# Kernel tuning notes

Measured on AMD Instinct MI355X. Metric: run time of the kernel, lower is better.

The kernel has to match this reference:

```python
import jax, jax.numpy as jnp
import numpy as np

IN_DIM, EDGE_DIM, HID = 128, 64, 128
N_A, N_B, E_AB, E_AA = 50000, 50000, 320000, 320000


def setup_inputs() -> dict:
    key = jax.random.key(0)
    ks = jax.random.split(key, 13)
    inv = lambda n: 1.0 / np.sqrt(n)
    return {
        "x_a": jax.random.normal(ks[0], (N_A, IN_DIM), jnp.float32),
        "x_b": jax.random.normal(ks[1], (N_B, IN_DIM), jnp.float32),
        "ei_ab": jax.random.randint(ks[2], (2, E_AB), 0, N_A),
        "ea_ab": jax.random.normal(ks[3], (E_AB, EDGE_DIM), jnp.float32),
        "ei_aa": jax.random.randint(ks[4], (2, E_AA), 0, N_A),
        "ea_aa": jax.random.normal(ks[5], (E_AA, EDGE_DIM), jnp.float32),
        "Wh_w": jax.random.normal(ks[6], (EDGE_DIM, HID), jnp.float32) * inv(EDGE_DIM),
        "Wh_b": jnp.zeros((HID,), jnp.float32),
        "Wn_w": jax.random.normal(ks[7], (2 * IN_DIM, HID), jnp.float32) * inv(2 * IN_DIM),
        "Wn_b": jnp.zeros((HID,), jnp.float32),
        "w_e": jax.random.normal(ks[8], (HID,), jnp.float32) * inv(HID),
        "ft_w": jax.random.normal(ks[9], (IN_DIM, IN_DIM), jnp.float32) * inv(IN_DIM),
        "ft_b": jnp.zeros((IN_DIM,), jnp.float32),
    }


def reference(x_a, x_b, ei_ab, ea_ab, ei_aa, ea_aa,
              Wh_w, Wh_b, Wn_w, Wn_b, w_e, ft_w, ft_b):
    def edge_alpha(x_src, x_dst, ei, ea):
        # gather src/dst feats -> linear + relu -> score -> softmax over all edges
        s, d = ei[0], ei[1]
        nf = jnp.concatenate([x_src[s], x_dst[d]], axis=1)          # [E, 2*in_dim]
        h = jax.nn.relu(ea @ Wh_w + Wh_b + nf @ Wn_w + Wn_b)         # [E, hid]
        return jax.nn.softmax(h @ w_e, axis=0)                       # [E]

    alpha_ab = edge_alpha(x_a, x_b, ei_ab, ea_ab)
    alpha_aa = edge_alpha(x_a, x_a, ei_aa, ea_aa)

    lf_a = jnp.zeros_like(x_a)
    lf_b = jnp.zeros_like(x_b)
    s_ab, d_ab = ei_ab[0], ei_ab[1]
    # cross-type edge: scatter into both endpoint node types
    lf_a = lf_a.at[s_ab].add(-alpha_ab[:, None] * x_b[d_ab])
    lf_b = lf_b.at[d_ab].add(-alpha_ab[:, None] * x_a[s_ab])
    s_aa, d_aa = ei_aa[0], ei_aa[1]
    # same-type edge: single scatter (src side only, per original)
    lf_a = lf_a.at[s_aa].add(-alpha_aa[:, None] * x_a[d_aa])

    out_a = x_a + lf_a
    out_a = out_a + (out_a @ ft_w + ft_b)
    out_b = x_b + lf_b
    out_b = out_b + (out_b @ ft_w + ft_b)
    return out_a, out_b, alpha_ab, alpha_aa
```

## Files before the change

### kernel.cpp

```cpp
#include <hip/hip_runtime.h>
#include <hip/hip_fp16.h>
#include <cstdint>
#include <cstddef>

#define N_A   50000
#define N_B   50000
#define E_AB  320000
#define E_AA  320000
#define IN_DIM 128
#define HID    128
#define ED     64

using bf16x8 = __attribute__((ext_vector_type(8))) short;
using f32x4  = __attribute__((ext_vector_type(4))) float;
typedef unsigned short ushort_t;
typedef unsigned int   uint_t;
typedef unsigned char  uchar_t;

#define X8_SCALE 0.0625f

__device__ inline ushort_t bf16r(float f) {
    uint_t u = __float_as_uint(f);
    u = (u + 0x7FFF + ((u >> 16) & 1)) >> 16;
    return (ushort_t)u;
}
__device__ inline float bf2f(ushort_t h) {
    return __uint_as_float(((uint_t)h) << 16);
}
__device__ inline ushort_t f16r(float f) { return __half_as_ushort(__float2half_rn(f)); }
__device__ inline float f16f(ushort_t u) { return __half2float(__ushort_as_half(u)); }
__device__ inline uint_t packh2(float a, float b) {
    return (uint_t)f16r(a) | ((uint_t)f16r(b) << 16);
}

__device__ inline uint_t enc_entry(int src, int flag, float score) {
    const uint_t h = (uint_t)f16r(score);
    return (uint_t)src | ((uint_t)flag << 16) | ((h & 0xFFFEu) << 16);
}

__device__ inline void online_merge(float& m, float& l, float om, float ol) {
    const float nm = fmaxf(m, om);
    l = l * __expf(m - nm) + ol * __expf(om - nm);
    m = nm;
}

__device__ inline uint_t pack_i8x4(float a, float b, float c, float d) {
    int q0 = __float2int_rn(a * 16.f); q0 = q0 < -127 ? -127 : (q0 > 127 ? 127 : q0);
    int q1 = __float2int_rn(b * 16.f); q1 = q1 < -127 ? -127 : (q1 > 127 ? 127 : q1);
    int q2 = __float2int_rn(c * 16.f); q2 = q2 < -127 ? -127 : (q2 > 127 ? 127 : q2);
    int q3 = __float2int_rn(d * 16.f); q3 = q3 < -127 ? -127 : (q3 > 127 ? 127 : q3);
    return (uint_t)(q0 & 0xFF) | ((uint_t)(q1 & 0xFF) << 8)
         | ((uint_t)(q2 & 0xFF) << 16) | ((uint_t)(q3 & 0xFF) << 24);
}

__global__ __launch_bounds__(64) void prep_w_all(
    const float* __restrict__ Wh, const float* __restrict__ W1,
    const float* __restrict__ W2, const float* __restrict__ FT,
    const float* __restrict__ we,
    ushort_t* __restrict__ BhWh, ushort_t* __restrict__ BlWh,
    ushort_t* __restrict__ BhW1, ushort_t* __restrict__ BlW1,
    ushort_t* __restrict__ BhW2, ushort_t* __restrict__ BlW2,
    ushort_t* __restrict__ BhFT, ushort_t* __restrict__ BlFT,
    float* __restrict__ wep)
{
    const int f = blockIdx.x;
    const int lane = threadIdx.x;
    if (f == 112) {
#pragma unroll
        for (int q = 0; q < 2; ++q) {
            const int idx = lane + q * 64;
            const int l15 = idx >> 3, ct = idx & 7;
            wep[idx] = we[ct * 16 + l15];
        }
        return;
    }
    const float* W; ushort_t *oh, *ol; int KT, fl;
    if (f < 16)      { W = Wh; oh = BhWh; ol = BlWh; KT = 2; fl = f; }
    else if (f < 48) { W = W1; oh = BhW1; ol = BlW1; KT = 4; fl = f - 16; }
    else if (f < 80) { W = W2; oh = BhW2; ol = BlW2; KT = 4; fl = f - 48; }
    else             { W = FT; oh = BhFT; ol = BlFT; KT = 4; fl = f - 80; }
    const int ct = fl / KT, kt = fl % KT;
    const int col = ct * 16 + (lane & 15);
    const int kb  = kt * 32 + (lane >> 4) * 8;
#pragma unroll
    for (int j = 0; j < 8; ++j) {
        const float v = W[(kb + j) * 128 + col];
        const ushort_t h = bf16r(v);
        oh[(size_t)(fl * 64 + lane) * 8 + j] = h;
        ol[(size_t)(fl * 64 + lane) * 8 + j] = bf16r(v - bf2f(h));
    }
}

__global__ __launch_bounds__(256) void proj_all_mfma(
    const float* __restrict__ x_a, const float* __restrict__ x_b,
    const ushort_t* __restrict__ B1h, const ushort_t* __restrict__ B1l,
    const ushort_t* __restrict__ B2h, const ushort_t* __restrict__ B2l,
    const float* __restrict__ bh, const float* __restrict__ bn,
    ushort_t* __restrict__ P1, ushort_t* __restrict__ P2a,
    ushort_t* __restrict__ P2b,
    uchar_t* __restrict__ xa8, uchar_t* __restrict__ xb8,
    int nblkA)
{
    const int lane = threadIdx.x & 63;
    const int l15 = lane & 15, lg = lane >> 4;
    const int isA = (blockIdx.x < nblkA);
    const int bb  = isA ? blockIdx.x : (blockIdx.x - nblkA);
    const int r0  = bb * 64 + (threadIdx.x >> 6) * 16;
    const int N   = isA ? N_A : N_B;
    const float* __restrict__ X = isA ? x_a : x_b;
    uchar_t* __restrict__ X8    = isA ? xa8 : xb8;
    const int arow = (r0 + l15 < N) ? (r0 + l15) : (N - 1);

    bf16x8 ahi[4], alo[4];
#pragma unroll
    for (int kt = 0; kt < 4; ++kt) {
        float v[8];
        *(float4*)(v + 0) = *(const float4*)&X[(size_t)arow * 128 + kt * 32 + lg * 8];
        *(float4*)(v + 4) = *(const float4*)&X[(size_t)arow * 128 + kt * 32 + lg * 8 + 4];
        uint2 xu;
        xu.x = pack_i8x4(v[0], v[1], v[2], v[3]);
        xu.y = pack_i8x4(v[4], v[5], v[6], v[7]);
        *(uint2*)&X8[(size_t)arow * 128 + kt * 32 + lg * 8] = xu;
#pragma unroll
        for (int j = 0; j < 8; ++j) {
            const ushort_t h = bf16r(v[j]);
            ahi[kt][j] = (short)h;
            alo[kt][j] = (short)bf16r(v[j] - bf2f(h));
        }
    }

    if (isA) {
        f32x4 acc1[8], acc2[8];
#pragma unroll
        for (int ct = 0; ct < 8; ++ct) {
            const float b = bh[ct * 16 + l15] + bn[ct * 16 + l15];
            acc1[ct] = (f32x4){b, b, b, b};
            acc2[ct] = (f32x4){0.f, 0.f, 0.f, 0.f};
        }
#pragma unroll
        for (int ct = 0; ct < 8; ++ct) {
#pragma unroll
            for (int kt = 0; kt < 4; ++kt) {
                const size_t fo = (size_t)((ct * 4 + kt) * 64 + lane) * 8;
                const bf16x8 b1h = *(const bf16x8*)&B1h[fo];
                const bf16x8 b1l = *(const bf16x8*)&B1l[fo];
                const bf16x8 b2h = *(const bf16x8*)&B2h[fo];
                const bf16x8 b2l = *(const bf16x8*)&B2l[fo];
                acc1[ct] = __builtin_amdgcn_mfma_f32_16x16x32_bf16(ahi[kt], b1h, acc1[ct], 0, 0, 0);
                acc1[ct] = __builtin_amdgcn_mfma_f32_16x16x32_bf16(alo[kt], b1h, acc1[ct], 0, 0, 0);
                acc1[ct] = __builtin_amdgcn_mfma_f32_16x16x32_bf16(ahi[kt], b1l, acc1[ct], 0, 0, 0);
                acc2[ct] = __builtin_amdgcn_mfma_f32_16x16x32_bf16(ahi[kt], b2h, acc2[ct], 0, 0, 0);
                acc2[ct] = __builtin_amdgcn_mfma_f32_16x16x32_bf16(alo[kt], b2h, acc2[ct], 0, 0, 0);
                acc2[ct] = __builtin_amdgcn_mfma_f32_16x16x32_bf16(ahi[kt], b2l, acc2[ct], 0, 0, 0);
            }
        }
#pragma unroll
        for (int i = 0; i < 4; ++i) {
            const int row = r0 + lg * 4 + i;
            if (row < N_A) {
                uint4 u1, u2;
                u1.x = packh2(acc1[0][i], acc1[1][i]); u1.y = packh2(acc1[2][i], acc1[3][i]);
                u1.z = packh2(acc1[4][i], acc1[5][i]); u1.w = packh2(acc1[6][i], acc1[7][i]);
                u2.x = packh2(acc2[0][i], acc2[1][i]); u2.y = packh2(acc2[2][i], acc2[3][i]);
                u2.z = packh2(acc2[4][i], acc2[5][i]); u2.w = packh2(acc2[6][i], acc2[7][i]);
                *(uint4*)&P1[(size_t)row * 128 + l15 * 8]  = u1;
                *(uint4*)&P2a[(size_t)row * 128 + l15 * 8] = u2;
            }
        }
    } else {
        f32x4 acc[8];
#pragma unroll
        for (int ct = 0; ct < 8; ++ct) acc[ct] = (f32x4){0.f, 0.f, 0.f, 0.f};
#pragma unroll
        for (int ct = 0; ct < 8; ++ct) {
#pragma unroll
            for (int kt = 0; kt < 4; ++kt) {
                const size_t fo = (size_t)((ct * 4 + kt) * 64 + lane) * 8;
                const bf16x8 bhf = *(const bf16x8*)&B2h[fo];
                const bf16x8 blf = *(const bf16x8*)&B2l[fo];
                acc[ct] = __builtin_amdgcn_mfma_f32_16x16x32_bf16(ahi[kt], bhf, acc[ct], 0, 0, 0);
                acc[ct] = __builtin_amdgcn_mfma_f32_16x16x32_bf16(alo[kt], bhf, acc[ct], 0, 0, 0);
                acc[ct] = __builtin_amdgcn_mfma_f32_16x16x32_bf16(ahi[kt], blf, acc[ct], 0, 0, 0);
            }
        }
#pragma unroll
        for (int i = 0; i < 4; ++i) {
            const int row = r0 + lg * 4 + i;
            if (row < N_B) {
                uint4 u;
                u.x = packh2(acc[0][i], acc[1][i]); u.y = packh2(acc[2][i], acc[3][i]);
                u.z = packh2(acc[4][i], acc[5][i]); u.w = packh2(acc[6][i], acc[7][i]);
                *(uint4*)&P2b[(size_t)row * 128 + l15 * 8] = u;
            }
        }
    }
}

__global__ __launch_bounds__(512) void edge_score_k(
    const float* __restrict__ ea_ab, const float* __restrict__ ea_aa,
    const int*   __restrict__ ei_ab, const int*   __restrict__ ei_aa,
    const ushort_t* __restrict__ P1h,
    const ushort_t* __restrict__ P2ah, const ushort_t* __restrict__ P2bh,
    const ushort_t* __restrict__ Bhi,  const ushort_t* __restrict__ Blo,
    const float* __restrict__ wep,
    float* __restrict__ scAB, float* __restrict__ scAA,
    int* __restrict__ cntA, int* __restrict__ cntB,
    uchar_t* __restrict__ rkAab, uchar_t* __restrict__ rkBab,
    uchar_t* __restrict__ rkAaa,
    float* __restrict__ pm, float* __restrict__ pl)
{
    const int t    = threadIdx.x;
    const int lane = t & 63;
    const int l15  = lane & 15;
    const int lg   = lane >> 4;
    const int wv   = t >> 6;
    const int type = (blockIdx.x >= 2500);
    const int bb   = type ? (blockIdx.x - 2500) : blockIdx.x;
    const int eb   = bb * 128;

    const float* __restrict__ ea  = type ? ea_aa : ea_ab;
    const int*   __restrict__ ei  = type ? ei_aa : ei_ab;
    const ushort_t* __restrict__ P2h = type ? P2ah : P2bh;
    float* __restrict__ score = type ? scAA : scAB;

    __shared__ ushort_t sBh[8192];
    __shared__ ushort_t sBl[8192];
    {
        const uint4* gh = (const uint4*)Bhi;
        const uint4* gl = (const uint4*)Blo;
        uint4* sh = (uint4*)sBh;
        uint4* sl = (uint4*)sBl;
#pragma unroll
        for (int i = 0; i < 2; ++i) {
            sh[t + i * 512] = gh[t + i * 512];
            sl[t + i * 512] = gl[t + i * 512];
        }
    }

    if (t < 128) {
        const int e = eb + t;
        const int s = ei[e];
        const int r = atomicAdd(&cntA[s], 1);
        if (type) rkAaa[e] = (uchar_t)r; else rkAab[e] = (uchar_t)r;
    } else if (t < 256 && !type) {
        const int e = eb + (t - 128);
        const int d = ei[(size_t)E_AB + e];
        rkBab[e] = (uchar_t)atomicAdd(&cntB[d], 1);
    }

    const int e0 = eb + wv * 16;

    const int4 sv = *(const int4*)&ei[e0 + lg * 4];
    const int4 dv = *(const int4*)&ei[(size_t)E_AB + e0 + lg * 4];
    const int sidx[4] = {sv.x, sv.y, sv.z, sv.w};
    const int didx[4] = {dv.x, dv.y, dv.z, dv.w};
    uint4 p1u[4], p2u[4];
#pragma unroll
    for (int i = 0; i < 4; ++i) {
        p1u[i] = *(const uint4*)&P1h[(size_t)sidx[i] * 128 + l15 * 8];
        p2u[i] = *(const uint4*)&P2h[(size_t)didx[i] * 128 + l15 * 8];
    }

    const float* arow = &ea[(size_t)(e0 + l15) * 64 + lg * 8];
    float af[16];
    *(float4*)(af + 0)  = *(const float4*)(arow + 0);
    *(float4*)(af + 4)  = *(const float4*)(arow + 4);
    *(float4*)(af + 8)  = *(const float4*)(arow + 32);
    *(float4*)(af + 12) = *(const float4*)(arow + 36);

    bf16x8 ahi0, alo0, ahi1, alo1;
#pragma unroll
    for (int j = 0; j < 8; ++j) {
        const ushort_t h0 = bf16r(af[j]);
        ahi0[j] = (short)h0;
        alo0[j] = (short)bf16r(af[j] - bf2f(h0));
        const ushort_t h1 = bf16r(af[8 + j]);
        ahi1[j] = (short)h1;
        alo1[j] = (short)bf16r(af[8 + j] - bf2f(h1));
    }

    __syncthreads();

    f32x4 acc[8];
#pragma unroll
    for (int ct = 0; ct < 8; ++ct) acc[ct] = (f32x4){0.f, 0.f, 0.f, 0.f};

#pragma unroll
    for (int ct = 0; ct < 8; ++ct) {
        const bf16x8 bh0 = *(const bf16x8*)&sBh[(ct * 2 + 0) * 512 + lane * 8];
        const bf16x8 bl0 = *(const bf16x8*)&sBl[(ct * 2 + 0) * 512 + lane * 8];
        const bf16x8 bh1 = *(const bf16x8*)&sBh[(ct * 2 + 1) * 512 + lane * 8];
        const bf16x8 bl1 = *(const bf16x8*)&sBl[(ct * 2 + 1) * 512 + lane * 8];
        acc[ct] = __builtin_amdgcn_mfma_f32_16x16x32_bf16(ahi0, bh0, acc[ct], 0, 0, 0);
        acc[ct] = __builtin_amdgcn_mfma_f32_16x16x32_bf16(alo0, bh0, acc[ct], 0, 0, 0);
        acc[ct] = __builtin_amdgcn_mfma_f32_16x16x32_bf16(ahi0, bl0, acc[ct], 0, 0, 0);
        acc[ct] = __builtin_amdgcn_mfma_f32_16x16x32_bf16(ahi1, bh1, acc[ct], 0, 0, 0);
        acc[ct] = __builtin_amdgcn_mfma_f32_16x16x32_bf16(alo1, bh1, acc[ct], 0, 0, 0);
        acc[ct] = __builtin_amdgcn_mfma_f32_16x16x32_bf16(ahi1, bl1, acc[ct], 0, 0, 0);
    }

    float w8[8];
    *(float4*)(w8 + 0) = *(const float4*)&wep[l15 * 8];
    *(float4*)(w8 + 4) = *(const float4*)&wep[l15 * 8 + 4];

    float part[4];
#pragma unroll
    for (int i = 0; i < 4; ++i) {
        const __half2* h1 = (const __half2*)&p1u[i];
        const __half2* h2 = (const __half2*)&p2u[i];
        float p = 0.f;
#pragma unroll
        for (int q = 0; q < 4; ++q) {
            const float2 pf = __half22float2(__hadd2(h1[q], h2[q]));
            p = fmaf(fmaxf(acc[2 * q][i] + pf.x, 0.f), w8[2 * q], p);
            p = fmaf(fmaxf(acc[2 * q + 1][i] + pf.y, 0.f), w8[2 * q + 1], p);
        }
        part[i] = p;
    }
#pragma unroll
    for (int m = 8; m >= 1; m >>= 1) {
#pragma unroll
        for (int i = 0; i < 4; ++i) part[i] += __shfl_xor(part[i], m, 64);
    }
    if (l15 == 0) {
#pragma unroll
        for (int i = 0; i < 4; ++i) score[e0 + lg * 4 + i] = part[i];
    }

    float mw = fmaxf(fmaxf(part[0], part[1]), fmaxf(part[2], part[3]));
    float lw = __expf(part[0] - mw) + __expf(part[1] - mw)
             + __expf(part[2] - mw) + __expf(part[3] - mw);
#pragma unroll
    for (int off = 16; off <= 32; off <<= 1) {
        const float om = __shfl_xor(mw, off, 64);
        const float ol = __shfl_xor(lw, off, 64);
        online_merge(mw, lw, om, ol);
    }
    __shared__ float smm[8], sll[8];
    if (lane == 0) { smm[wv] = mw; sll[wv] = lw; }
    __syncthreads();
    if (t == 0) {
        float M = smm[0], L = sll[0];
        for (int i = 1; i < 8; ++i) online_merge(M, L, smm[i], sll[i]);
        pm[blockIdx.x] = M;
        pl[blockIdx.x] = L;
    }
}

__global__ __launch_bounds__(1024) void softmax_scan_kernel(
    const float* __restrict__ pm, const float* __restrict__ pl,
    float* __restrict__ ML, int nPart,
    const int* __restrict__ cntA, int* __restrict__ offA,
    const int* __restrict__ cntB, int* __restrict__ offB, int N)
{
    const int t = threadIdx.x, lane = t & 63, w = t >> 6;

    if (blockIdx.x < 2) {
        const int type = blockIdx.x;
        const float* mi = pm + type * nPart;
        const float* li = pl + type * nPart;
        float m = -1e30f, l = 0.f;
        for (int i = t; i < nPart; i += 1024) online_merge(m, l, mi[i], li[i]);
#pragma unroll
        for (int off = 1; off < 64; off <<= 1) {
            const float om = __shfl_xor(m, off, 64);
            const float ol = __shfl_xor(l, off, 64);
            online_merge(m, l, om, ol);
        }
        __shared__ float smm[16], sll[16];
        if (lane == 0) { smm[w] = m; sll[w] = l; }
        __syncthreads();
        if (t == 0) {
            float M = smm[0], L = sll[0];
            for (int i = 1; i < 16; ++i) online_merge(M, L, smm[i], sll[i]);
            ML[type * 2]     = M;
            ML[type * 2 + 1] = L;
        }
    } else {
        const int* cnt = (blockIdx.x == 2) ? cntA : cntB;
        int* off = (blockIdx.x == 2) ? offA : offB;

        __shared__ int warpsum[16];
        int carry = 0;
        for (int base = 0; base < N; base += 1024) {
            const int i = base + t;
            const int v = (i < N) ? cnt[i] : 0;
            int x = v;
#pragma unroll
            for (int d = 1; d < 64; d <<= 1) {
                const int y = __shfl_up(x, d, 64);
                if (lane >= d) x += y;
            }
            if (lane == 63) warpsum[w] = x;
            __syncthreads();
            if (w == 0 && lane < 16) {
                int s = warpsum[lane];
#pragma unroll
                for (int d = 1; d < 16; d <<= 1) {
                    const int y = __shfl_up(s, d, 64);
                    if (lane >= d) s += y;
                }
                warpsum[lane] = s;
            }
            __syncthreads();
            const int excl = (x - v) + ((w > 0) ? warpsum[w - 1] : 0) + carry;
            if (i < N) off[i] = excl;
            carry += warpsum[15];
            __syncthreads();
        }
        if (t == 0) off[N] = carry;
    }
}

__global__ __launch_bounds__(256) void csr_fill_kernel(
    const int* __restrict__ ei_ab, const int* __restrict__ ei_aa,
    float* __restrict__ scAB, float* __restrict__ scAA,
    const float* __restrict__ ML,
    const int* __restrict__ offA, const int* __restrict__ offB,
    const uchar_t* __restrict__ rkAab, const uchar_t* __restrict__ rkBab,
    const uchar_t* __restrict__ rkAaa,
    uint_t* __restrict__ idxA, uint_t* __restrict__ idxB)
{
    const int i = blockIdx.x * 256 + threadIdx.x;
    const float Mab = ML[0], rLab = 1.0f / ML[1];
    const float Maa = ML[2], rLaa = 1.0f / ML[3];
    if (i < E_AB) {
        const float sraw = scAB[i];
        scAB[i] = __expf(sraw - Mab) * rLab;
        const int s = ei_ab[i], d = ei_ab[E_AB + i];
        int pA = offA[s] + rkAab[i]; if (pA > 2 * E_AB - 1) pA = 2 * E_AB - 1;
        int pB = offB[d] + rkBab[i]; if (pB > E_AB - 1) pB = E_AB - 1;
        idxA[pA] = enc_entry(d, 1, sraw);
        idxB[pB] = enc_entry(s, 0, sraw);
    }
    if (i < E_AA) {
        const float sraw = scAA[i];
        scAA[i] = __expf(sraw - Maa) * rLaa;
        const int s = ei_aa[i];
        const int daa = ei_aa[E_AA + i];
        int pA = offA[s] + rkAaa[i]; if (pA > 2 * E_AB - 1) pA = 2 * E_AB - 1;
        idxA[pA] = enc_entry(daa, 0, sraw);
    }
}

__device__ inline void accum_i8(float a8[8], float als, uint2 f) {
    a8[0] = fmaf(als, (float)(char)(f.x),       a8[0]);
    a8[1] = fmaf(als, (float)(char)(f.x >> 8),  a8[1]);
    a8[2] = fmaf(als, (float)(char)(f.x >> 16), a8[2]);
    a8[3] = fmaf(als, (float)(char)(f.x >> 24), a8[3]);
    a8[4] = fmaf(als, (float)(char)(f.y),       a8[4]);
    a8[5] = fmaf(als, (float)(char)(f.y >> 8),  a8[5]);
    a8[6] = fmaf(als, (float)(char)(f.y >> 16), a8[6]);
    a8[7] = fmaf(als, (float)(char)(f.y >> 24), a8[7]);
}

__global__ __launch_bounds__(256) void gather_all(
    const int* __restrict__ offA, const uint_t* __restrict__ idxA,
    const int* __restrict__ offB, const uint_t* __restrict__ idxB,
    const uchar_t* __restrict__ xa8, const uchar_t* __restrict__ xb8,
    const float* __restrict__ ML,
    const float* __restrict__ x_a, const float* __restrict__ x_b,
    const ushort_t* __restrict__ Bh, const ushort_t* __restrict__ Bl,
    const float* __restrict__ fb,
    float* __restrict__ TA, float* __restrict__ TB, int nblkA)
{
    const int lane = threadIdx.x & 63;
    const int l15  = lane & 15, lg = lane >> 4;
    const int wv   = threadIdx.x >> 6;
    const int isA  = (blockIdx.x < nblkA);
    const int bb   = isA ? blockIdx.x : (blockIdx.x - nblkA);
    const int r0   = bb * 64 + wv * 16;
    const int N    = isA ? N_A : N_B;

    const int*    __restrict__ off = isA ? offA : offB;
    const uint_t* __restrict__ idx = isA ? idxA : idxB;
    const float*  __restrict__ xself = isA ? x_a : x_b;
    float* __restrict__ T = isA ? TA : TB;

    const float M0  = isA ? ML[2] : ML[0];
    const float rL0 = 1.0f / (isA ? ML[3] : ML[1]);
    const float M1  = ML[0];
    const float rL1 = 1.0f / ML[1];

    for (int s = 0; s < 4; ++s) {
        const int row = r0 + s * 4 + lg;
        if (row < N) {
            const int beg = off[row], end = off[row + 1];
            float a8[8];
            *(float4*)(a8 + 0) = *(const float4*)&xself[(size_t)row * 128 + l15 * 8];
            *(float4*)(a8 + 4) = *(const float4*)&xself[(size_t)row * 128 + l15 * 8 + 4];
            int e = beg;
            for (; e + 7 < end; e += 8) {
                uint_t v[8];
#pragma unroll
                for (int k = 0; k < 8; ++k) v[k] = idx[e + k];
                uint2 f[8];
#pragma unroll
                for (int k = 0; k < 8; ++k) {
                    const uchar_t* sp = (v[k] & 0x10000u) ? xb8 : xa8;
                    f[k] = *(const uint2*)&sp[(size_t)(v[k] & 0xFFFFu) * 128 + l15 * 8];
                }
#pragma unroll
                for (int k = 0; k < 8; ++k) {
                    const int fl = (v[k] >> 16) & 1;
                    const float sc = f16f((ushort_t)((v[k] >> 16) & 0xFFFEu));
                    const float al = __expf(sc - (fl ? M1 : M0)) * (fl ? rL1 : rL0);
                    accum_i8(a8, -al * X8_SCALE, f[k]);
                }
            }
            for (; e < end; ++e) {
                const uint_t v = idx[e];
                const uchar_t* sp = (v & 0x10000u) ? xb8 : xa8;
                const uint2 f0 = *(const uint2*)&sp[(size_t)(v & 0xFFFFu) * 128 + l15 * 8];
                const int fl = (v >> 16) & 1;
                const float sc = f16f((ushort_t)((v >> 16) & 0xFFFEu));
                const float al = __expf(sc - (fl ? M1 : M0)) * (fl ? rL1 : rL0);
                accum_i8(a8, -al * X8_SCALE, f0);
            }
            *(float4*)&T[(size_t)row * 128 + l15 * 8]     = *(float4*)(a8 + 0);
            *(float4*)&T[(size_t)row * 128 + l15 * 8 + 4] = *(float4*)(a8 + 4);
        }
    }
    __syncthreads();

    const int arow = (r0 + l15 < N) ? (r0 + l15) : (N - 1);
    bf16x8 ahi[4], alo[4];
#pragma unroll
    for (int kt = 0; kt < 4; ++kt) {
        float v[8];
        *(float4*)(v + 0) = *(const float4*)&T[(size_t)arow * 128 + kt * 32 + lg * 8];
        *(float4*)(v + 4) = *(const float4*)&T[(size_t)arow * 128 + kt * 32 + lg * 8 + 4];
#pragma unroll
        for (int j = 0; j < 8; ++j) {
            const ushort_t h = bf16r(v[j]);
            ahi[kt][j] = (short)h;
            alo[kt][j] = (short)bf16r(v[j] - bf2f(h));
        }
    }

    f32x4 acc[8];
#pragma unroll
    for (int ct = 0; ct < 8; ++ct) {
        const float b = fb[ct * 16 + l15];
#pragma unroll
        for (int i = 0; i < 4; ++i) {
            const int row = r0 + lg * 4 + i;
            const int rr = (row < N) ? row : (N - 1);
            acc[ct][i] = T[(size_t)rr * 128 + ct * 16 + l15] + b;
        }
    }

#pragma unroll
    for (int ct = 0; ct < 8; ++ct) {
#pragma unroll
        for (int kt = 0; kt < 4; ++kt) {
            const size_t fo = (size_t)((ct * 4 + kt) * 64 + lane) * 8;
            const bf16x8 bhf = *(const bf16x8*)&Bh[fo];
            const bf16x8 blf = *(const bf16x8*)&Bl[fo];
            acc[ct] = __builtin_amdgcn_mfma_f32_16x16x32_bf16(ahi[kt], bhf, acc[ct], 0, 0, 0);
            acc[ct] = __builtin_amdgcn_mfma_f32_16x16x32_bf16(alo[kt], bhf, acc[ct], 0, 0, 0);
            acc[ct] = __builtin_amdgcn_mfma_f32_16x16x32_bf16(ahi[kt], blf, acc[ct], 0, 0, 0);
        }
    }
#pragma unroll
    for (int ct = 0; ct < 8; ++ct) {
#pragma unroll
        for (int i = 0; i < 4; ++i) {
            const int row = r0 + lg * 4 + i;
            if (row < N) T[(size_t)row * 128 + ct * 16 + l15] = acc[ct][i];
        }
    }
}

extern "C" void kernel_launch(void* const* d_in, const int* in_sizes, int n_in,
                              void* d_out, int out_size, void* d_ws, size_t ws_size,
                              hipStream_t stream)
{
    const float* x_a   = (const float*)d_in[0];
    const float* x_b   = (const float*)d_in[1];
    const int*   ei_ab = (const int*)d_in[2];
    const float* ea_ab = (const float*)d_in[3];
    const int*   ei_aa = (const int*)d_in[4];
    const float* ea_aa = (const float*)d_in[5];
    const float* Wh_w  = (const float*)d_in[6];
    const float* Wh_b  = (const float*)d_in[7];
    const float* Wn_w  = (const float*)d_in[8];
    const float* Wn_b  = (const float*)d_in[9];
    const float* w_e   = (const float*)d_in[10];
    const float* ft_w  = (const float*)d_in[11];
    const float* ft_b  = (const float*)d_in[12];

    float* out = (float*)d_out;
    float* ws  = (float*)d_ws;

    ushort_t* P1h  = (ushort_t*)(ws);
    ushort_t* P2ah = (ushort_t*)(ws + 3200000);
    ushort_t* P2bh = (ushort_t*)(ws + 6400000);
    uchar_t*  xa8  = (uchar_t*)(ws + 9600000);
    uchar_t*  xb8  = (uchar_t*)(ws + 11200000);
    uchar_t* rkAab = (uchar_t*)(ws + 16000000);
    uchar_t* rkBab = (uchar_t*)(ws + 16080000);
    uchar_t* rkAaa = (uchar_t*)(ws + 16160000);
    int* cntA  = (int*)(ws + 16960000);
    int* cntB  = (int*)(ws + 17010000);
    int* offA  = (int*)(ws + 17060000);
    int* offB  = (int*)(ws + 17110004);
    float* pm  = ws + 17160008;
    float* pl  = ws + 17165008;
    float* ML  = ws + 17170008;
    float* wep = ws + 17170016;
    ushort_t* FR = (ushort_t*)(ws + 17170208);
    ushort_t* BhWh = FR;
    ushort_t* BlWh = FR + 8192;
    ushort_t* BhW1 = FR + 16384;
    ushort_t* BlW1 = FR + 32768;
    ushort_t* BhW2 = FR + 49152;
    ushort_t* BlW2 = FR + 65536;
    ushort_t* BhFT = FR + 81920;
    ushort_t* BlFT = FR + 98304;
    uint_t* idxA = (uint_t*)(ws + 17230000);
    uint_t* idxB = (uint_t*)(ws + 17870000);

    float* TA   = out;
    float* TB   = out + 6400000;
    float* alAB = out + 12800000;
    float* alAA = out + 13120000;

    const int nblkA = (N_A + 63) / 64;
    const int nblkB = (N_B + 63) / 64;

    hipMemsetAsync(cntA, 0, 100000 * sizeof(int), stream);
    prep_w_all<<<113, 64, 0, stream>>>(Wh_w, Wn_w, Wn_w + 128 * 128, ft_w, w_e,
                                       BhWh, BlWh, BhW1, BlW1, BhW2, BlW2, BhFT, BlFT, wep);

    proj_all_mfma<<<nblkA + nblkB, 256, 0, stream>>>(x_a, x_b,
                                                     BhW1, BlW1, BhW2, BlW2,
                                                     Wh_b, Wn_b,
                                                     P1h, P2ah, P2bh, xa8, xb8, nblkA);

    edge_score_k<<<5000, 512, 0, stream>>>(ea_ab, ea_aa, ei_ab, ei_aa,
                                           P1h, P2ah, P2bh, BhWh, BlWh, wep,
                                           alAB, alAA, cntA, cntB,
                                           rkAab, rkBab, rkAaa, pm, pl);

    softmax_scan_kernel<<<4, 1024, 0, stream>>>(pm, pl, ML, 2500,
                                                cntA, offA, cntB, offB, N_A);

    csr_fill_kernel<<<(E_AB + 255) / 256, 256, 0, stream>>>(ei_ab, ei_aa, alAB, alAA, ML,
                                                            offA, offB, rkAab, rkBab, rkAaa,
                                                            idxA, idxB);

    gather_all<<<nblkA + nblkB, 256, 0, stream>>>(offA, idxA, offB, idxB,
                                                  xa8, xb8, ML, x_a, x_b,
                                                  BhFT, BlFT, ft_b, TA, TB, nblkA);

    (void)in_sizes; (void)n_in; (void)out_size; (void)ws_size;
}
```

Measured before the change: 302.0 us.

## Split gather from final matmul and store prescaled alpha in CSR entries

The fused gather+GEMM kernel is split into two. The first is a gather-only kernel that gives each 16-lane group one row, uses a finer grid and drops the block-wide barrier. The second is a separate kernel that applies the ft_w transform. CSR entries now carry the softmax-normalized alpha, scaled by 1024 and stored as fp16, instead of the raw score, so the per-edge exp and max/sum lookup leave the gather loop. The trade-off is an extra kernel launch, a round trip of T through global memory, and a change in fp16 quantization of the weights.

```diff
diff --git a/kernel.cpp b/kernel.cpp
--- a/kernel.cpp
+++ b/kernel.cpp
@@ -18,6 +18,7 @@
 typedef unsigned char  uchar_t;
 
 #define X8_SCALE 0.0625f
+#define AL_SCALE 1024.0f
 
 __device__ inline ushort_t bf16r(float f) {
     uint_t u = __float_as_uint(f);
@@ -33,8 +34,8 @@
     return (uint_t)f16r(a) | ((uint_t)f16r(b) << 16);
 }
 
-__device__ inline uint_t enc_entry(int src, int flag, float score) {
-    const uint_t h = (uint_t)f16r(score);
+__device__ inline uint_t enc_entry(int src, int flag, float alpha_s) {
+    const uint_t h = (uint_t)f16r(alpha_s);
     return (uint_t)src | ((uint_t)flag << 16) | ((h & 0xFFFEu) << 16);
 }
 
@@ -425,21 +426,21 @@
     const float Mab = ML[0], rLab = 1.0f / ML[1];
     const float Maa = ML[2], rLaa = 1.0f / ML[3];
     if (i < E_AB) {
-        const float sraw = scAB[i];
-        scAB[i] = __expf(sraw - Mab) * rLab;
+        const float a = __expf(scAB[i] - Mab) * rLab;
+        scAB[i] = a;
         const int s = ei_ab[i], d = ei_ab[E_AB + i];
         int pA = offA[s] + rkAab[i]; if (pA > 2 * E_AB - 1) pA = 2 * E_AB - 1;
         int pB = offB[d] + rkBab[i]; if (pB > E_AB - 1) pB = E_AB - 1;
-        idxA[pA] = enc_entry(d, 1, sraw);
-        idxB[pB] = enc_entry(s, 0, sraw);
+        idxA[pA] = enc_entry(d, 1, a * AL_SCALE);
+        idxB[pB] = enc_entry(s, 0, a * AL_SCALE);
     }
     if (i < E_AA) {
-        const float sraw = scAA[i];
-        scAA[i] = __expf(sraw - Maa) * rLaa;
+        const float a = __expf(scAA[i] - Maa) * rLaa;
+        scAA[i] = a;
         const int s = ei_aa[i];
         const int daa = ei_aa[E_AA + i];
         int pA = offA[s] + rkAaa[i]; if (pA > 2 * E_AB - 1) pA = 2 * E_AB - 1;
-        idxA[pA] = enc_entry(daa, 0, sraw);
+        idxA[pA] = enc_entry(daa, 0, a * AL_SCALE);
     }
 }
 
@@ -454,12 +455,61 @@
     a8[7] = fmaf(als, (float)(char)(f.y >> 24), a8[7]);
 }
 
-__global__ __launch_bounds__(256) void gather_all(
+__global__ __launch_bounds__(256) void gather_only(
     const int* __restrict__ offA, const uint_t* __restrict__ idxA,
     const int* __restrict__ offB, const uint_t* __restrict__ idxB,
     const uchar_t* __restrict__ xa8, const uchar_t* __restrict__ xb8,
-    const float* __restrict__ ML,
     const float* __restrict__ x_a, const float* __restrict__ x_b,
+    float* __restrict__ TA, float* __restrict__ TB, int nblkAg)
+{
+    const int l15 = threadIdx.x & 15;
+    const int qw  = threadIdx.x >> 4;
+    const int isA = (blockIdx.x < nblkAg);
+    const int bb  = isA ? blockIdx.x : (blockIdx.x - nblkAg);
+    const int row = bb * 16 + qw;
+    const int N   = isA ? N_A : N_B;
+    if (row >= N) return;
+
+    const int*    __restrict__ off = isA ? offA : offB;
+    const uint_t* __restrict__ idx = isA ? idxA : idxB;
+    const float*  __restrict__ xself = isA ? x_a : x_b;
+    float* __restrict__ T = isA ? TA : TB;
+
+    const int beg = off[row], end = off[row + 1];
+    float a8[8];
+    *(float4*)(a8 + 0) = *(const float4*)&xself[(size_t)row * 128 + l15 * 8];
+    *(float4*)(a8 + 4) = *(const float4*)&xself[(size_t)row * 128 + l15 * 8 + 4];
+
+    const float KQ = X8_SCALE / AL_SCALE;
+    int e = beg;
+    for (; e + 7 < end; e += 8) {
+        uint_t v[8];
+#pragma unroll
+        for (int k = 0; k < 8; ++k) v[k] = idx[e + k];
+        uint2 f[8];
+#pragma unroll
+        for (int k = 0; k < 8; ++k) {
+            const uchar_t* sp = (v[k] & 0x10000u) ? xb8 : xa8;
+            f[k] = *(const uint2*)&sp[(size_t)(v[k] & 0xFFFFu) * 128 + l15 * 8];
+        }
+#pragma unroll
+        for (int k = 0; k < 8; ++k) {
+            const float al = f16f((ushort_t)((v[k] >> 16) & 0xFFFEu));
+            accum_i8(a8, -al * KQ, f[k]);
+        }
+    }
+    for (; e < end; ++e) {
+        const uint_t v = idx[e];
+        const uchar_t* sp = (v & 0x10000u) ? xb8 : xa8;
+        const uint2 f0 = *(const uint2*)&sp[(size_t)(v & 0xFFFFu) * 128 + l15 * 8];
+        const float al = f16f((ushort_t)((v >> 16) & 0xFFFEu));
+        accum_i8(a8, -al * KQ, f0);
+    }
+    *(float4*)&T[(size_t)row * 128 + l15 * 8]     = *(float4*)(a8 + 0);
+    *(float4*)&T[(size_t)row * 128 + l15 * 8 + 4] = *(float4*)(a8 + 4);
+}
+
+__global__ __launch_bounds__(256) void final_all(
     const ushort_t* __restrict__ Bh, const ushort_t* __restrict__ Bl,
     const float* __restrict__ fb,
     float* __restrict__ TA, float* __restrict__ TB, int nblkA)
@@ -471,57 +521,7 @@
     const int bb   = isA ? blockIdx.x : (blockIdx.x - nblkA);
     const int r0   = bb * 64 + wv * 16;
     const int N    = isA ? N_A : N_B;
-
-    const int*    __restrict__ off = isA ? offA : offB;
-    const uint_t* __restrict__ idx = isA ? idxA : idxB;
-    const float*  __restrict__ xself = isA ? x_a : x_b;
     float* __restrict__ T = isA ? TA : TB;
-
-    const float M0  = isA ? ML[2] : ML[0];
-    const float rL0 = 1.0f / (isA ? ML[3] : ML[1]);
-    const float M1  = ML[0];
-    const float rL1 = 1.0f / ML[1];
-
-    for (int s = 0; s < 4; ++s) {
-        const int row = r0 + s * 4 + lg;
-        if (row < N) {
-            const int beg = off[row], end = off[row + 1];
-            float a8[8];
-            *(float4*)(a8 + 0) = *(const float4*)&xself[(size_t)row * 128 + l15 * 8];
-            *(float4*)(a8 + 4) = *(const float4*)&xself[(size_t)row * 128 + l15 * 8 + 4];
-            int e = beg;
-            for (; e + 7 < end; e += 8) {
-                uint_t v[8];
-#pragma unroll
-                for (int k = 0; k < 8; ++k) v[k] = idx[e + k];
-                uint2 f[8];
-#pragma unroll
-                for (int k = 0; k < 8; ++k) {
-                    const uchar_t* sp = (v[k] & 0x10000u) ? xb8 : xa8;
-                    f[k] = *(const uint2*)&sp[(size_t)(v[k] & 0xFFFFu) * 128 + l15 * 8];
-                }
-#pragma unroll
-                for (int k = 0; k < 8; ++k) {
-                    const int fl = (v[k] >> 16) & 1;
-                    const float sc = f16f((ushort_t)((v[k] >> 16) & 0xFFFEu));
-                    const float al = __expf(sc - (fl ? M1 : M0)) * (fl ? rL1 : rL0);
-                    accum_i8(a8, -al * X8_SCALE, f[k]);
-                }
-            }
-            for (; e < end; ++e) {
-                const uint_t v = idx[e];
-                const uchar_t* sp = (v & 0x10000u) ? xb8 : xa8;
-                const uint2 f0 = *(const uint2*)&sp[(size_t)(v & 0xFFFFu) * 128 + l15 * 8];
-                const int fl = (v >> 16) & 1;
-                const float sc = f16f((ushort_t)((v >> 16) & 0xFFFEu));
-                const float al = __expf(sc - (fl ? M1 : M0)) * (fl ? rL1 : rL0);
-                accum_i8(a8, -al * X8_SCALE, f0);
-            }
-            *(float4*)&T[(size_t)row * 128 + l15 * 8]     = *(float4*)(a8 + 0);
-            *(float4*)&T[(size_t)row * 128 + l15 * 8 + 4] = *(float4*)(a8 + 4);
-        }
-    }
-    __syncthreads();
 
     const int arow = (r0 + l15 < N) ? (r0 + l15) : (N - 1);
     bf16x8 ahi[4], alo[4];
@@ -626,8 +626,10 @@
     float* alAB = out + 12800000;
     float* alAA = out + 13120000;
 
-    const int nblkA = (N_A + 63) / 64;
-    const int nblkB = (N_B + 63) / 64;
+    const int nblkA  = (N_A + 63) / 64;
+    const int nblkB  = (N_B + 63) / 64;
+    const int nblkAg = (N_A + 15) / 16;
+    const int nblkBg = (N_B + 15) / 16;
 
     hipMemsetAsync(cntA, 0, 100000 * sizeof(int), stream);
     prep_w_all<<<113, 64, 0, stream>>>(Wh_w, Wn_w, Wn_w + 128 * 128, ft_w, w_e,
@@ -650,9 +652,11 @@
                                                             offA, offB, rkAab, rkBab, rkAaa,
                                                             idxA, idxB);
 
-    gather_all<<<nblkA + nblkB, 256, 0, stream>>>(offA, idxA, offB, idxB,
-                                                  xa8, xb8, ML, x_a, x_b,
-                                                  BhFT, BlFT, ft_b, TA, TB, nblkA);
+    gather_only<<<nblkAg + nblkBg, 256, 0, stream>>>(offA, idxA, offB, idxB,
+                                                     xa8, xb8, x_a, x_b,
+                                                     TA, TB, nblkAg);
+
+    final_all<<<nblkA + nblkB, 256, 0, stream>>>(BhFT, BlFT, ft_b, TA, TB, nblkA);
 
     (void)in_sizes; (void)n_in; (void)out_size; (void)ws_size;
 }
```

Measured after the change: 293.3 us. 1.03x faster.
